# Performance work log

Measured on AMD Instinct MI355X. Metric: run time of the kernel, lower is better.

## Reference

```python
import jax, jax.numpy as jnp
import numpy as np

N, E = 20000, 320000
IN, HID, OUT, H = 128, 32, 1, 4
EPS = 1e-16  # PyG softmax epsilon


def _p(key, shape, scale=0.05):
    return jax.random.normal(key, shape, dtype=jnp.float32) * scale


def setup_inputs() -> dict:
    key = jax.random.key(0)
    ks = jax.random.split(key, 20)
    d = {
        "x": jax.random.normal(ks[0], (N, IN), dtype=jnp.float32),
        "edge_src": jax.random.randint(ks[1], (E,), 0, N, dtype=jnp.int32),
        "edge_dst": jax.random.randint(ks[2], (E,), 0, N, dtype=jnp.int32),
        # layer 1: TransformerConv(IN, HID, H)  ->  [N, H*HID]
        "W1q": _p(ks[3], (IN, H * HID)), "b1q": jnp.zeros((H * HID,), jnp.float32),
        "W1k": _p(ks[4], (IN, H * HID)), "b1k": jnp.zeros((H * HID,), jnp.float32),
        "W1v": _p(ks[5], (IN, H * HID)), "b1v": jnp.zeros((H * HID,), jnp.float32),
        "W1s": _p(ks[6], (IN, H * HID)), "b1s": jnp.zeros((H * HID,), jnp.float32),
        # layer 2: TransformerConv(H*HID, OUT, H) -> [N, H*OUT]
        "W2q": _p(ks[7], (H * HID, H * OUT)), "b2q": jnp.zeros((H * OUT,), jnp.float32),
        "W2k": _p(ks[8], (H * HID, H * OUT)), "b2k": jnp.zeros((H * OUT,), jnp.float32),
        "W2v": _p(ks[9], (H * HID, H * OUT)), "b2v": jnp.zeros((H * OUT,), jnp.float32),
        "W2s": _p(ks[10], (H * HID, H * OUT)), "b2s": jnp.zeros((H * OUT,), jnp.float32),
        # final nn.Linear(heads, 1)
        "Wl": _p(ks[11], (H, 1)), "bl": jnp.zeros((1,), jnp.float32),
    }
    return d


def transformer_conv(x, src, dst, Wq, bq, Wk, bk, Wv, bv, Ws, bs, heads, ch):
    n = x.shape[0]
    q = (x @ Wq + bq).reshape(n, heads, ch)
    k = (x @ Wk + bk).reshape(n, heads, ch)
    v = (x @ Wv + bv).reshape(n, heads, ch)
    qi, kj, vj = q[dst], k[src], v[src]            # [E,H,C] gathers
    score = (qi * kj).sum(-1) / jnp.sqrt(jnp.float32(ch))  # [E,H]
    m = jax.ops.segment_max(score, dst, num_segments=n)    # segment softmax by target
    e = jnp.exp(score - m[dst])
    s = jax.ops.segment_sum(e, dst, num_segments=n)
    alpha = e / (s[dst] + EPS)                              # [E,H]
    agg = jax.ops.segment_sum(alpha[:, :, None] * vj, dst, num_segments=n)  # [N,H,C]
    return agg.reshape(n, heads * ch) + x @ Ws + bs          # concat + root skip


def reference(x, edge_src, edge_dst,
              W1q, b1q, W1k, b1k, W1v, b1v, W1s, b1s,
              W2q, b2q, W2k, b2k, W2v, b2v, W2s, b2s,
              Wl, bl):
    h = transformer_conv(x, edge_src, edge_dst, W1q, b1q, W1k, b1k, W1v, b1v, W1s, b1s, H, HID)
    h = jax.nn.relu(h)  # dropout is identity in eval
    h = transformer_conv(h, edge_src, edge_dst, W2q, b2q, W2k, b2k, W2v, b2v, W2s, b2s, H, OUT)
    y = h @ Wl + bl                      # [N,1]
    return y.mean(axis=0, keepdims=True)  # [1,1]
```

## Files before the change

### kernel.cpp

```cpp
#include <hip/hip_runtime.h>
#include <math.h>

static constexpr float EPS_PYG = 1e-16f;
static constexpr float INV_SQRT32 = 0.17677669529663687f;
static constexpr int CAP = 64;
static constexpr int CAP_SH = 6;

typedef short bf16x8 __attribute__((ext_vector_type(8)));
typedef float f32x4 __attribute__((ext_vector_type(4)));

__device__ inline unsigned short f2bf(float f) {
    union { float f; unsigned u; } x; x.f = f;
    unsigned r = x.u + 0x7FFFu + ((x.u >> 16) & 1u);
    return (unsigned short)(r >> 16);
}
__device__ inline float bf_hi(unsigned u) {
    union { unsigned u; float f; } x; x.u = u & 0xFFFF0000u; return x.f;
}
__device__ inline float bf_lo(unsigned u) {
    union { unsigned u; float f; } x; x.u = u << 16; return x.f;
}

__global__ __launch_bounds__(256) void build_csr_kernel(
    const int* __restrict__ src, const int* __restrict__ dst,
    int* __restrict__ deg, int* __restrict__ csr_src,
    int E, int nblk_deg,
    const float* __restrict__ Wq, const float* __restrict__ Wk,
    const float* __restrict__ Wv, const float* __restrict__ Wsk,
    unsigned short* __restrict__ Wbt,
    float* __restrict__ out, const float* __restrict__ bl)
{
    const int b = blockIdx.x;
    const int t = threadIdx.x;
    if (b < nblk_deg) {
        const int e0 = b * 1024 + t;
        const int e1 = e0 + 256, e2 = e0 + 512, e3 = e0 + 768;
        const bool v0 = e0 < E, v1 = e1 < E, v2 = e2 < E, v3 = e3 < E;
        int d0 = 0, d1 = 0, d2 = 0, d3 = 0;
        int s0 = 0, s1 = 0, s2 = 0, s3 = 0;
        if (v0) { d0 = dst[e0]; s0 = src[e0]; }
        if (v1) { d1 = dst[e1]; s1 = src[e1]; }
        if (v2) { d2 = dst[e2]; s2 = src[e2]; }
        if (v3) { d3 = dst[e3]; s3 = src[e3]; }
        int sl0 = 0, sl1 = 0, sl2 = 0, sl3 = 0;
        if (v0) sl0 = atomicAdd(&deg[d0], 1);
        if (v1) sl1 = atomicAdd(&deg[d1], 1);
        if (v2) sl2 = atomicAdd(&deg[d2], 1);
        if (v3) sl3 = atomicAdd(&deg[d3], 1);
        if (v0 && sl0 < CAP) csr_src[(d0 << CAP_SH) + sl0] = s0;
        if (v1 && sl1 < CAP) csr_src[(d1 << CAP_SH) + sl1] = s1;
        if (v2 && sl2 < CAP) csr_src[(d2 << CAP_SH) + sl2] = s2;
        if (v3 && sl3 < CAP) csr_src[(d3 << CAP_SH) + sl3] = s3;
    } else if (b < nblk_deg + 4) {
        int m = b - nblk_deg;
        const float* W = (m == 0) ? Wq : (m == 1) ? Wk : (m == 2) ? Wv : Wsk;
        for (int i = t; i < 16384; i += 256) {
            int k = i >> 7, nn = i & 127;
            Wbt[(m << 14) + nn * 128 + k] = f2bf(W[i]);
        }
    } else {
        if (t == 0) out[0] = bl[0];
    }
}

__global__ __launch_bounds__(256) void gemm1_mfma(
    const float* __restrict__ X, const unsigned short* __restrict__ Wbt,
    const float* __restrict__ bq, const float* __restrict__ bk,
    const float* __restrict__ bv, const float* __restrict__ bsk,
    unsigned int* __restrict__ QS, unsigned int* __restrict__ KV, int n)
{
    const int mode  = blockIdx.y >> 1;
    const int chalf = blockIdx.y & 1;

    const int tid  = threadIdx.x;
    const int wave = tid >> 6;
    const int lane = tid & 63;
    const int m    = lane & 15;
    const int quad = lane >> 4;
    const int r0   = blockIdx.x * 64 + wave * 16;

    int arow = r0 + m;
    if (arow >= n) arow = n - 1;

    const float4* xr = (const float4*)(X + (size_t)arow * 128);

    bf16x8 afr[4];
#pragma unroll
    for (int kc4 = 0; kc4 < 4; ++kc4) {
        float4 f0 = xr[kc4 * 8 + quad * 2];
        float4 f1 = xr[kc4 * 8 + quad * 2 + 1];
        bf16x8 a;
        a[0] = (short)f2bf(f0.x); a[1] = (short)f2bf(f0.y);
        a[2] = (short)f2bf(f0.z); a[3] = (short)f2bf(f0.w);
        a[4] = (short)f2bf(f1.x); a[5] = (short)f2bf(f1.y);
        a[6] = (short)f2bf(f1.z); a[7] = (short)f2bf(f1.w);
        afr[kc4] = a;
    }

    const unsigned short* WA = Wbt + (size_t)(mode ? 1 : 0) * 16384;
    const unsigned short* WB = Wbt + (size_t)(mode ? 2 : 3) * 16384;
    const float* biasA = mode ? bk : bq;
    const float* biasB = mode ? bv : bsk;
    unsigned int* Out = mode ? KV : QS;

    f32x4 accA[4] = {};
    f32x4 accB[4] = {};
#pragma unroll
    for (int kc4 = 0; kc4 < 4; ++kc4) {
        const int koff = kc4 * 32 + quad * 8;
#pragma unroll
        for (int c = 0; c < 4; ++c) {
            const int ct = chalf * 4 + c;
            bf16x8 ba = *(const bf16x8*)(WA + (ct * 16 + m) * 128 + koff);
            accA[c] = __builtin_amdgcn_mfma_f32_16x16x32_bf16(afr[kc4], ba, accA[c], 0, 0, 0);
            bf16x8 bb = *(const bf16x8*)(WB + (ct * 16 + m) * 128 + koff);
            accB[c] = __builtin_amdgcn_mfma_f32_16x16x32_bf16(afr[kc4], bb, accB[c], 0, 0, 0);
        }
    }
#pragma unroll
    for (int c = 0; c < 4; ++c) {
        const int col = (chalf * 4 + c) * 16 + m;
        const float bA = biasA[col], bB = biasB[col];
#pragma unroll
        for (int r = 0; r < 4; ++r) {
            const int row = r0 + quad * 4 + r;
            if (row < n) {
                unsigned ha = f2bf(accA[c][r] + bA);
                unsigned lb = f2bf(accB[c][r] + bB);
                Out[(size_t)row * 128 + col] = (ha << 16) | lb;
            }
        }
    }
}

__global__ __launch_bounds__(256) void l1_agg_kernel(
    const unsigned int* __restrict__ QS, const unsigned int* __restrict__ KV,
    const int* __restrict__ deg, const int* __restrict__ csr_src,
    const float* __restrict__ W2q, const float* __restrict__ W2k,
    const float* __restrict__ W2v, const float* __restrict__ W2s,
    const float* __restrict__ b2q, const float* __restrict__ b2k,
    const float* __restrict__ b2v, const float* __restrict__ b2s,
    float4* __restrict__ Q2, float4* __restrict__ KV2, float4* __restrict__ S2,
    int n)
{
    const int t = threadIdx.x;
    const int node = blockIdx.x * 4 + (t >> 6);
    if (node >= n) return;
    const int l    = t & 31;
    const int half = (t >> 5) & 1;
    const int lf   = t & 63;
    const int cbase = ((l >> 3) << 5) + ((l & 7) << 2);

    const int beg = node << CAP_SH;
    int cnt = deg[node]; if (cnt > CAP) cnt = CAP;

    const int eall = csr_src[beg + lf];

    const uint4 qs = *(const uint4*)(QS + (size_t)node * 128 + cbase);
    const float4 q = make_float4(bf_hi(qs.x), bf_hi(qs.y), bf_hi(qs.z), bf_hi(qs.w));

    float lsum = 0.f, a0 = 0.f, a1 = 0.f, a2 = 0.f, a3 = 0.f;
    int p_base = 0;
    for (; p_base + 8 <= cnt; p_base += 8) {
        const int p = p_base + half;
        int s0 = __shfl(eall, p, 64);
        int s1 = __shfl(eall, p + 2, 64);
        int s2 = __shfl(eall, p + 4, 64);
        int s3 = __shfl(eall, p + 6, 64);
        uint4 u0 = *(const uint4*)(KV + (size_t)s0 * 128 + cbase);
        uint4 u1 = *(const uint4*)(KV + (size_t)s1 * 128 + cbase);
        uint4 u2 = *(const uint4*)(KV + (size_t)s2 * 128 + cbase);
        uint4 u3 = *(const uint4*)(KV + (size_t)s3 * 128 + cbase);
        float p0 = q.x * bf_hi(u0.x) + q.y * bf_hi(u0.y)
                 + q.z * bf_hi(u0.z) + q.w * bf_hi(u0.w);
        float p1 = q.x * bf_hi(u1.x) + q.y * bf_hi(u1.y)
                 + q.z * bf_hi(u1.z) + q.w * bf_hi(u1.w);
        float p2 = q.x * bf_hi(u2.x) + q.y * bf_hi(u2.y)
                 + q.z * bf_hi(u2.z) + q.w * bf_hi(u2.w);
        float p3 = q.x * bf_hi(u3.x) + q.y * bf_hi(u3.y)
                 + q.z * bf_hi(u3.z) + q.w * bf_hi(u3.w);
        p0 += __shfl_xor(p0, 4, 8);  p1 += __shfl_xor(p1, 4, 8);
        p2 += __shfl_xor(p2, 4, 8);  p3 += __shfl_xor(p3, 4, 8);
        p0 += __shfl_xor(p0, 2, 8);  p1 += __shfl_xor(p1, 2, 8);
        p2 += __shfl_xor(p2, 2, 8);  p3 += __shfl_xor(p3, 2, 8);
        p0 += __shfl_xor(p0, 1, 8);  p1 += __shfl_xor(p1, 1, 8);
        p2 += __shfl_xor(p2, 1, 8);  p3 += __shfl_xor(p3, 1, 8);
        float e0 = __expf(p0 * INV_SQRT32);
        float e1 = __expf(p1 * INV_SQRT32);
        float e2 = __expf(p2 * INV_SQRT32);
        float e3 = __expf(p3 * INV_SQRT32);
        lsum += (e0 + e1) + (e2 + e3);
        a0 += e0 * bf_lo(u0.x) + e1 * bf_lo(u1.x)
            + e2 * bf_lo(u2.x) + e3 * bf_lo(u3.x);
        a1 += e0 * bf_lo(u0.y) + e1 * bf_lo(u1.y)
            + e2 * bf_lo(u2.y) + e3 * bf_lo(u3.y);
        a2 += e0 * bf_lo(u0.z) + e1 * bf_lo(u1.z)
            + e2 * bf_lo(u2.z) + e3 * bf_lo(u3.z);
        a3 += e0 * bf_lo(u0.w) + e1 * bf_lo(u1.w)
            + e2 * bf_lo(u2.w) + e3 * bf_lo(u3.w);
    }
    if (p_base < cnt) {
        const int pclamp = cnt - 1;
#pragma unroll
        for (int j = 0; j < 4; ++j) {
            int p = p_base + half + 2 * j;
            const bool valid = p < cnt;
            int ps = valid ? p : pclamp;
            int s0 = __shfl(eall, ps, 64);
            uint4 u0 = *(const uint4*)(KV + (size_t)s0 * 128 + cbase);
            float p0 = q.x * bf_hi(u0.x) + q.y * bf_hi(u0.y)
                     + q.z * bf_hi(u0.z) + q.w * bf_hi(u0.w);
            p0 += __shfl_xor(p0, 4, 8);
            p0 += __shfl_xor(p0, 2, 8);
            p0 += __shfl_xor(p0, 1, 8);
            float e0 = valid ? __expf(p0 * INV_SQRT32) : 0.f;
            lsum += e0;
            a0 += e0 * bf_lo(u0.x);
            a1 += e0 * bf_lo(u0.y);
            a2 += e0 * bf_lo(u0.z);
            a3 += e0 * bf_lo(u0.w);
        }
    }
    lsum += __shfl_xor(lsum, 32, 64);
    a0   += __shfl_xor(a0,   32, 64);
    a1   += __shfl_xor(a1,   32, 64);
    a2   += __shfl_xor(a2,   32, 64);
    a3   += __shfl_xor(a3,   32, 64);

    const float inv = 1.0f / (lsum + EPS_PYG);
    const float h0 = fmaxf(a0 * inv + bf_lo(qs.x), 0.f);
    const float h1 = fmaxf(a1 * inv + bf_lo(qs.y), 0.f);
    const float h2 = fmaxf(a2 * inv + bf_lo(qs.z), 0.f);
    const float h3 = fmaxf(a3 * inv + bf_lo(qs.w), 0.f);

    const float* WA = half ? W2v : W2q;
    const float* WB = half ? W2s : W2k;
    float p0, p1, p2, p3, p4, p5, p6, p7;
    {
        float4 wa = *(const float4*)(WA + (size_t)(cbase + 0) * 4);
        float4 wb = *(const float4*)(WB + (size_t)(cbase + 0) * 4);
        p0 = h0 * wa.x; p1 = h0 * wa.y; p2 = h0 * wa.z; p3 = h0 * wa.w;
        p4 = h0 * wb.x; p5 = h0 * wb.y; p6 = h0 * wb.z; p7 = h0 * wb.w;
        wa = *(const float4*)(WA + (size_t)(cbase + 1) * 4);
        wb = *(const float4*)(WB + (size_t)(cbase + 1) * 4);
        p0 += h1 * wa.x; p1 += h1 * wa.y; p2 += h1 * wa.z; p3 += h1 * wa.w;
        p4 += h1 * wb.x; p5 += h1 * wb.y; p6 += h1 * wb.z; p7 += h1 * wb.w;
        wa = *(const float4*)(WA + (size_t)(cbase + 2) * 4);
        wb = *(const float4*)(WB + (size_t)(cbase + 2) * 4);
        p0 += h2 * wa.x; p1 += h2 * wa.y; p2 += h2 * wa.z; p3 += h2 * wa.w;
        p4 += h2 * wb.x; p5 += h2 * wb.y; p6 += h2 * wb.z; p7 += h2 * wb.w;
        wa = *(const float4*)(WA + (size_t)(cbase + 3) * 4);
        wb = *(const float4*)(WB + (size_t)(cbase + 3) * 4);
        p0 += h3 * wa.x; p1 += h3 * wa.y; p2 += h3 * wa.z; p3 += h3 * wa.w;
        p4 += h3 * wb.x; p5 += h3 * wb.y; p6 += h3 * wb.z; p7 += h3 * wb.w;
    }
#pragma unroll
    for (int mk = 16; mk >= 1; mk >>= 1) {
        p0 += __shfl_xor(p0, mk, 32); p1 += __shfl_xor(p1, mk, 32);
        p2 += __shfl_xor(p2, mk, 32); p3 += __shfl_xor(p3, mk, 32);
        p4 += __shfl_xor(p4, mk, 32); p5 += __shfl_xor(p5, mk, 32);
        p6 += __shfl_xor(p6, mk, 32); p7 += __shfl_xor(p7, mk, 32);
    }
    if (lf == 0) {
        const float4 ba = *(const float4*)b2q;
        const float4 bb = *(const float4*)b2k;
        Q2[node] = make_float4(p0 + ba.x, p1 + ba.y, p2 + ba.z, p3 + ba.w);
        KV2[(size_t)node * 2 + 0] =
            make_float4(p4 + bb.x, p5 + bb.y, p6 + bb.z, p7 + bb.w);
    } else if (lf == 32) {
        const float4 ba = *(const float4*)b2v;
        const float4 bb = *(const float4*)b2s;
        KV2[(size_t)node * 2 + 1] =
            make_float4(p0 + ba.x, p1 + ba.y, p2 + ba.z, p3 + ba.w);
        S2[node] = make_float4(p4 + bb.x, p5 + bb.y, p6 + bb.z, p7 + bb.w);
    }
}

__global__ __launch_bounds__(256) void l2_agg_kernel(
    const float4* __restrict__ Q2, const float4* __restrict__ KV2,
    const float4* __restrict__ S2,
    const int* __restrict__ deg, const int* __restrict__ csr_src,
    const float* __restrict__ Wl, float* __restrict__ out, int n, float invn)
{
    const int t  = threadIdx.x;
    const int g  = t >> 4;
    const int gl = t & 15;
    const int nd = blockIdx.x * 16 + g;
    float y = 0.f;
    if (nd < n) {
        const int beg = nd << CAP_SH;
        int cnt = deg[nd]; if (cnt > CAP) cnt = CAP;
        const int end = beg + cnt;
        float4 q = Q2[nd];
        float l0 = 0.f, l1 = 0.f, l2 = 0.f, l3 = 0.f;
        float a0 = 0.f, a1 = 0.f, a2 = 0.f, a3 = 0.f;
        for (int pos = beg + gl; pos < end; pos += 16) {
            int src = csr_src[pos];
            float4 k = KV2[(size_t)src * 2 + 0];
            float4 v = KV2[(size_t)src * 2 + 1];
            float e0 = __expf(q.x * k.x);
            float e1 = __expf(q.y * k.y);
            float e2 = __expf(q.z * k.z);
            float e3 = __expf(q.w * k.w);
            l0 += e0; a0 += e0 * v.x;
            l1 += e1; a1 += e1 * v.y;
            l2 += e2; a2 += e2 * v.z;
            l3 += e3; a3 += e3 * v.w;
        }
#pragma unroll
        for (int mk = 8; mk >= 1; mk >>= 1) {
            l0 += __shfl_xor(l0, mk, 16); l1 += __shfl_xor(l1, mk, 16);
            l2 += __shfl_xor(l2, mk, 16); l3 += __shfl_xor(l3, mk, 16);
            a0 += __shfl_xor(a0, mk, 16); a1 += __shfl_xor(a1, mk, 16);
            a2 += __shfl_xor(a2, mk, 16); a3 += __shfl_xor(a3, mk, 16);
        }
        if (gl == 0) {
            float4 sk = S2[nd];
            float h0 = a0 / (l0 + EPS_PYG) + sk.x;
            float h1 = a1 / (l1 + EPS_PYG) + sk.y;
            float h2 = a2 / (l2 + EPS_PYG) + sk.z;
            float h3 = a3 / (l3 + EPS_PYG) + sk.w;
            y = (h0 * Wl[0] + h1 * Wl[1] + h2 * Wl[2] + h3 * Wl[3]) * invn;
        }
    }
    __shared__ float red[256];
    red[t] = y;
    __syncthreads();
    for (int off = 128; off > 0; off >>= 1) {
        if (t < (unsigned)off) red[t] += red[t + off];
        __syncthreads();
    }
    if (t == 0) atomicAdd(out, red[0]);
}

extern "C" void kernel_launch(void* const* d_in, const int* in_sizes, int n_in,
                              void* d_out, int out_size, void* d_ws, size_t ws_size,
                              hipStream_t stream) {
    const float* x        = (const float*)d_in[0];
    const int*   edge_src = (const int*)d_in[1];
    const int*   edge_dst = (const int*)d_in[2];
    const float* W1q = (const float*)d_in[3];  const float* b1q = (const float*)d_in[4];
    const float* W1k = (const float*)d_in[5];  const float* b1k = (const float*)d_in[6];
    const float* W1v = (const float*)d_in[7];  const float* b1v = (const float*)d_in[8];
    const float* W1s = (const float*)d_in[9];  const float* b1s = (const float*)d_in[10];
    const float* W2q = (const float*)d_in[11]; const float* b2q = (const float*)d_in[12];
    const float* W2k = (const float*)d_in[13]; const float* b2k = (const float*)d_in[14];
    const float* W2v = (const float*)d_in[15]; const float* b2v = (const float*)d_in[16];
    const float* W2s = (const float*)d_in[17]; const float* b2s = (const float*)d_in[18];
    const float* Wl  = (const float*)d_in[19]; const float* bl  = (const float*)d_in[20];

    const int N = in_sizes[0] / 128;
    const int E = in_sizes[1];
    float* out = (float*)d_out;

    float* ws  = (float*)d_ws;
    size_t off = 0;
    unsigned int* QS  = (unsigned int*)(ws + off); off += (size_t)N * 128;
    unsigned int* KV  = (unsigned int*)(ws + off); off += (size_t)N * 128;
    float*        q2  = ws + off; off += (size_t)N * 4;
    float*        kv2 = ws + off; off += (size_t)N * 8;
    float*        s2  = ws + off; off += (size_t)N * 4;
    unsigned short* Wbt = (unsigned short*)(ws + off); off += 4 * 16384 / 2;
    int* deg     = (int*)(ws + off);
    int* csr_src = deg + N;

    const int nblk_e4 = (E + 1023) / 1024;
    const int nblk_g  = (N + 63) / 64;

    hipMemsetAsync(deg, 0, (size_t)N * sizeof(int), stream);
    build_csr_kernel<<<nblk_e4 + 5, 256, 0, stream>>>(
        edge_src, edge_dst, deg, csr_src, E, nblk_e4,
        W1q, W1k, W1v, W1s, Wbt, out, bl);
    {
        dim3 grid(nblk_g, 4);
        gemm1_mfma<<<grid, 256, 0, stream>>>(x, Wbt, b1q, b1k, b1v, b1s,
                                             QS, KV, N);
    }
    l1_agg_kernel<<<(N + 3) / 4, 256, 0, stream>>>(
        QS, KV, deg, csr_src, W2q, W2k, W2v, W2s, b2q, b2k, b2v, b2s,
        (float4*)q2, (float4*)kv2, (float4*)s2, N);
    l2_agg_kernel<<<(N + 15) / 16, 256, 0, stream>>>((const float4*)q2,
                                                     (const float4*)kv2,
                                                     (const float4*)s2,
                                                     deg, csr_src, Wl, out, N,
                                                     1.0f / (float)N);
}
```

Before: 208.7 us.

## Replace memset with init kernel, unroll l1 gathers by 16, flatten l2 loop

Replaces the hipMemsetAsync of the degree array with a zeroing init kernel that also does the weight bf16 transpose, leaving the CSR build as its own kernel. Adds a 16-neighbor unrolled path in the layer-1 aggregation so eight KV gathers are in flight per lane. Rewrites the layer-2 aggregation as a fixed four-slot predicated unroll over the 64-entry capacity, issuing all gathers up front. This trades a memset and loop overhead for extra registers and an extra kernel launch.

```diff
diff --git a/kernel.cpp b/kernel.cpp
--- a/kernel.cpp
+++ b/kernel.cpp
@@ -21,10 +21,8 @@
     union { unsigned u; float f; } x; x.u = u << 16; return x.f;
 }
 
-__global__ __launch_bounds__(256) void build_csr_kernel(
-    const int* __restrict__ src, const int* __restrict__ dst,
-    int* __restrict__ deg, int* __restrict__ csr_src,
-    int E, int nblk_deg,
+__global__ __launch_bounds__(256) void init_kernel(
+    int* __restrict__ deg, int N, int nblk_z,
     const float* __restrict__ Wq, const float* __restrict__ Wk,
     const float* __restrict__ Wv, const float* __restrict__ Wsk,
     unsigned short* __restrict__ Wbt,
@@ -32,27 +30,11 @@
 {
     const int b = blockIdx.x;
     const int t = threadIdx.x;
-    if (b < nblk_deg) {
-        const int e0 = b * 1024 + t;
-        const int e1 = e0 + 256, e2 = e0 + 512, e3 = e0 + 768;
-        const bool v0 = e0 < E, v1 = e1 < E, v2 = e2 < E, v3 = e3 < E;
-        int d0 = 0, d1 = 0, d2 = 0, d3 = 0;
-        int s0 = 0, s1 = 0, s2 = 0, s3 = 0;
-        if (v0) { d0 = dst[e0]; s0 = src[e0]; }
-        if (v1) { d1 = dst[e1]; s1 = src[e1]; }
-        if (v2) { d2 = dst[e2]; s2 = src[e2]; }
-        if (v3) { d3 = dst[e3]; s3 = src[e3]; }
-        int sl0 = 0, sl1 = 0, sl2 = 0, sl3 = 0;
-        if (v0) sl0 = atomicAdd(&deg[d0], 1);
-        if (v1) sl1 = atomicAdd(&deg[d1], 1);
-        if (v2) sl2 = atomicAdd(&deg[d2], 1);
-        if (v3) sl3 = atomicAdd(&deg[d3], 1);
-        if (v0 && sl0 < CAP) csr_src[(d0 << CAP_SH) + sl0] = s0;
-        if (v1 && sl1 < CAP) csr_src[(d1 << CAP_SH) + sl1] = s1;
-        if (v2 && sl2 < CAP) csr_src[(d2 << CAP_SH) + sl2] = s2;
-        if (v3 && sl3 < CAP) csr_src[(d3 << CAP_SH) + sl3] = s3;
-    } else if (b < nblk_deg + 4) {
-        int m = b - nblk_deg;
+    if (b < nblk_z) {
+        int i = b * 256 + t;
+        if (i < N) deg[i] = 0;
+    } else if (b < nblk_z + 4) {
+        int m = b - nblk_z;
         const float* W = (m == 0) ? Wq : (m == 1) ? Wk : (m == 2) ? Wv : Wsk;
         for (int i = t; i < 16384; i += 256) {
             int k = i >> 7, nn = i & 127;
@@ -61,6 +43,32 @@
     } else {
         if (t == 0) out[0] = bl[0];
     }
+}
+
+__global__ __launch_bounds__(256) void build_csr_kernel(
+    const int* __restrict__ src, const int* __restrict__ dst,
+    int* __restrict__ deg, int* __restrict__ csr_src, int E)
+{
+    const int b = blockIdx.x;
+    const int t = threadIdx.x;
+    const int e0 = b * 1024 + t;
+    const int e1 = e0 + 256, e2 = e0 + 512, e3 = e0 + 768;
+    const bool v0 = e0 < E, v1 = e1 < E, v2 = e2 < E, v3 = e3 < E;
+    int d0 = 0, d1 = 0, d2 = 0, d3 = 0;
+    int s0 = 0, s1 = 0, s2 = 0, s3 = 0;
+    if (v0) { d0 = dst[e0]; s0 = src[e0]; }
+    if (v1) { d1 = dst[e1]; s1 = src[e1]; }
+    if (v2) { d2 = dst[e2]; s2 = src[e2]; }
+    if (v3) { d3 = dst[e3]; s3 = src[e3]; }
+    int sl0 = 0, sl1 = 0, sl2 = 0, sl3 = 0;
+    if (v0) sl0 = atomicAdd(&deg[d0], 1);
+    if (v1) sl1 = atomicAdd(&deg[d1], 1);
+    if (v2) sl2 = atomicAdd(&deg[d2], 1);
+    if (v3) sl3 = atomicAdd(&deg[d3], 1);
+    if (v0 && sl0 < CAP) csr_src[(d0 << CAP_SH) + sl0] = s0;
+    if (v1 && sl1 < CAP) csr_src[(d1 << CAP_SH) + sl1] = s1;
+    if (v2 && sl2 < CAP) csr_src[(d2 << CAP_SH) + sl2] = s2;
+    if (v3 && sl3 < CAP) csr_src[(d3 << CAP_SH) + sl3] = s3;
 }
 
 __global__ __launch_bounds__(256) void gemm1_mfma(
@@ -161,6 +169,36 @@
 
     float lsum = 0.f, a0 = 0.f, a1 = 0.f, a2 = 0.f, a3 = 0.f;
     int p_base = 0;
+    for (; p_base + 16 <= cnt; p_base += 16) {
+        const int p = p_base + half;
+        int s[8];
+#pragma unroll
+        for (int j = 0; j < 8; ++j) s[j] = __shfl(eall, p + 2 * j, 64);
+        uint4 u[8];
+#pragma unroll
+        for (int j = 0; j < 8; ++j)
+            u[j] = *(const uint4*)(KV + (size_t)s[j] * 128 + cbase);
+        float pd[8];
+#pragma unroll
+        for (int j = 0; j < 8; ++j)
+            pd[j] = q.x * bf_hi(u[j].x) + q.y * bf_hi(u[j].y)
+                  + q.z * bf_hi(u[j].z) + q.w * bf_hi(u[j].w);
+#pragma unroll
+        for (int j = 0; j < 8; ++j) {
+            pd[j] += __shfl_xor(pd[j], 4, 8);
+            pd[j] += __shfl_xor(pd[j], 2, 8);
+            pd[j] += __shfl_xor(pd[j], 1, 8);
+        }
+#pragma unroll
+        for (int j = 0; j < 8; ++j) {
+            float e = __expf(pd[j] * INV_SQRT32);
+            lsum += e;
+            a0 += e * bf_lo(u[j].x);
+            a1 += e * bf_lo(u[j].y);
+            a2 += e * bf_lo(u[j].z);
+            a3 += e * bf_lo(u[j].w);
+        }
+    }
     for (; p_base + 8 <= cnt; p_base += 8) {
         const int p = p_base + half;
         int s0 = __shfl(eall, p, 64);
@@ -290,22 +328,52 @@
     if (nd < n) {
         const int beg = nd << CAP_SH;
         int cnt = deg[nd]; if (cnt > CAP) cnt = CAP;
-        const int end = beg + cnt;
+        const bool v0 = gl < cnt, v1 = gl + 16 < cnt,
+                   v2 = gl + 32 < cnt, v3 = gl + 48 < cnt;
+        int i0 = csr_src[beg + gl];
+        int i1 = csr_src[beg + gl + 16];
+        int i2 = csr_src[beg + gl + 32];
+        int i3 = csr_src[beg + gl + 48];
+        i0 = v0 ? i0 : 0; i1 = v1 ? i1 : 0;
+        i2 = v2 ? i2 : 0; i3 = v3 ? i3 : 0;
+        float4 k0 = KV2[(size_t)i0 * 2 + 0], w0 = KV2[(size_t)i0 * 2 + 1];
+        float4 k1 = KV2[(size_t)i1 * 2 + 0], w1 = KV2[(size_t)i1 * 2 + 1];
+        float4 k2 = KV2[(size_t)i2 * 2 + 0], w2 = KV2[(size_t)i2 * 2 + 1];
+        float4 k3 = KV2[(size_t)i3 * 2 + 0], w3 = KV2[(size_t)i3 * 2 + 1];
         float4 q = Q2[nd];
         float l0 = 0.f, l1 = 0.f, l2 = 0.f, l3 = 0.f;
         float a0 = 0.f, a1 = 0.f, a2 = 0.f, a3 = 0.f;
-        for (int pos = beg + gl; pos < end; pos += 16) {
-            int src = csr_src[pos];
-            float4 k = KV2[(size_t)src * 2 + 0];
-            float4 v = KV2[(size_t)src * 2 + 1];
-            float e0 = __expf(q.x * k.x);
-            float e1 = __expf(q.y * k.y);
-            float e2 = __expf(q.z * k.z);
-            float e3 = __expf(q.w * k.w);
-            l0 += e0; a0 += e0 * v.x;
-            l1 += e1; a1 += e1 * v.y;
-            l2 += e2; a2 += e2 * v.z;
-            l3 += e3; a3 += e3 * v.w;
+        {
+            float e0 = v0 ? __expf(q.x * k0.x) : 0.f;
+            float e1 = v0 ? __expf(q.y * k0.y) : 0.f;
+            float e2 = v0 ? __expf(q.z * k0.z) : 0.f;
+            float e3 = v0 ? __expf(q.w * k0.w) : 0.f;
+            l0 += e0; a0 += e0 * w0.x;  l1 += e1; a1 += e1 * w0.y;
+            l2 += e2; a2 += e2 * w0.z;  l3 += e3; a3 += e3 * w0.w;
+        }
+        {
+            float e0 = v1 ? __expf(q.x * k1.x) : 0.f;
+            float e1 = v1 ? __expf(q.y * k1.y) : 0.f;
+            float e2 = v1 ? __expf(q.z * k1.z) : 0.f;
+            float e3 = v1 ? __expf(q.w * k1.w) : 0.f;
+            l0 += e0; a0 += e0 * w1.x;  l1 += e1; a1 += e1 * w1.y;
+            l2 += e2; a2 += e2 * w1.z;  l3 += e3; a3 += e3 * w1.w;
+        }
+        {
+            float e0 = v2 ? __expf(q.x * k2.x) : 0.f;
+            float e1 = v2 ? __expf(q.y * k2.y) : 0.f;
+            float e2 = v2 ? __expf(q.z * k2.z) : 0.f;
+            float e3 = v2 ? __expf(q.w * k2.w) : 0.f;
+            l0 += e0; a0 += e0 * w2.x;  l1 += e1; a1 += e1 * w2.y;
+            l2 += e2; a2 += e2 * w2.z;  l3 += e3; a3 += e3 * w2.w;
+        }
+        {
+            float e0 = v3 ? __expf(q.x * k3.x) : 0.f;
+            float e1 = v3 ? __expf(q.y * k3.y) : 0.f;
+            float e2 = v3 ? __expf(q.z * k3.z) : 0.f;
+            float e3 = v3 ? __expf(q.w * k3.w) : 0.f;
+            l0 += e0; a0 += e0 * w3.x;  l1 += e1; a1 += e1 * w3.y;
+            l2 += e2; a2 += e2 * w3.z;  l3 += e3; a3 += e3 * w3.w;
         }
 #pragma unroll
         for (int mk = 8; mk >= 1; mk >>= 1) {
@@ -364,13 +432,14 @@
     int* deg     = (int*)(ws + off);
     int* csr_src = deg + N;
 
+    const int nblk_z  = (N + 255) / 256;
     const int nblk_e4 = (E + 1023) / 1024;
     const int nblk_g  = (N + 63) / 64;
 
-    hipMemsetAsync(deg, 0, (size_t)N * sizeof(int), stream);
-    build_csr_kernel<<<nblk_e4 + 5, 256, 0, stream>>>(
-        edge_src, edge_dst, deg, csr_src, E, nblk_e4,
-        W1q, W1k, W1v, W1s, Wbt, out, bl);
+    init_kernel<<<nblk_z + 5, 256, 0, stream>>>(
+        deg, N, nblk_z, W1q, W1k, W1v, W1s, Wbt, out, bl);
+    build_csr_kernel<<<nblk_e4, 256, 0, stream>>>(
+        edge_src, edge_dst, deg, csr_src, E);
     {
         dim3 grid(nblk_g, 4);
         gemm1_mfma<<<grid, 256, 0, stream>>>(x, Wbt, b1q, b1k, b1v, b1s,
```

Result: slower. 215.9 us (+3.4%).
